# Optimization experiments

Measured on AMD Instinct MI355X. Metric: run time of the kernel, lower is better.

The kernel has to match this reference:

```python
import jax, jax.numpy as jnp
import numpy as np

B, S, D = 4, 2048, 1024
H = 16
DH = D // H  # dim_q = dim_k = 64
F = 4096
EPS = 1e-5


def setup_inputs() -> dict:
    key = jax.random.key(0)
    ks = jax.random.split(key, 16)
    sd = 0.02
    inp = {
        'x': jax.random.normal(ks[0], (B, S, D), jnp.float32),
        'wq': jax.random.normal(ks[1], (H, D, DH), jnp.float32) * sd,
        'bq': jnp.zeros((H, DH), jnp.float32),
        'wk': jax.random.normal(ks[2], (H, D, DH), jnp.float32) * sd,
        'bk': jnp.zeros((H, DH), jnp.float32),
        'wv': jax.random.normal(ks[3], (H, D, DH), jnp.float32) * sd,
        'bv': jnp.zeros((H, DH), jnp.float32),
        'wo': jax.random.normal(ks[4], (H * DH, D), jnp.float32) * sd,
        'bo': jnp.zeros((D,), jnp.float32),
        'ln1_g': jnp.ones((D,), jnp.float32),
        'ln1_b': jnp.zeros((D,), jnp.float32),
        'w1': jax.random.normal(ks[5], (D, F), jnp.float32) * sd,
        'b1': jnp.zeros((F,), jnp.float32),
        'w2': jax.random.normal(ks[6], (F, D), jnp.float32) * sd,
        'b2': jnp.zeros((D,), jnp.float32),
        'ln2_g': jnp.ones((D,), jnp.float32),
        'ln2_b': jnp.zeros((D,), jnp.float32),
    }
    return inp


def _layernorm(x, g, b):
    mu = jnp.mean(x, axis=-1, keepdims=True)
    var = jnp.mean(jnp.square(x - mu), axis=-1, keepdims=True)
    return (x - mu) * jax.lax.rsqrt(var + EPS) * g + b


def _encoder_layer(x, wq, bq, wk, bk, wv, bv, wo, bo, ln1_g, ln1_b,
                   w1, b1, w2, b2, ln2_g, ln2_b):
    # Multi-head attention (all heads batched via einsum)
    q = jnp.einsum('bsd,hde->bhse', x, wq) + bq[:, None, :]
    k = jnp.einsum('bsd,hde->bhse', x, wk) + bk[:, None, :]
    v = jnp.einsum('bsd,hde->bhse', x, wv) + bv[:, None, :]
    scores = jnp.einsum('bhqe,bhke->bhqk', q, k) / jnp.sqrt(jnp.float32(DH))
    p = jax.nn.softmax(scores, axis=-1)
    o = jnp.einsum('bhqk,bhke->bhqe', p, v)  # [B,H,S,DH]
    o = o.transpose(0, 2, 1, 3).reshape(B, S, H * DH)  # concat heads
    attn = o @ wo + bo
    y = _layernorm(x + attn, ln1_g, ln1_b)  # post-norm residual
    # Feed-forward
    ff = jax.nn.relu(y @ w1 + b1) @ w2 + b2
    return _layernorm(y + ff, ln2_g, ln2_b)


def reference(x, wq, bq, wk, bk, wv, bv, wo, bo, ln1_g, ln1_b,
              w1, b1, w2, b2, ln2_g, ln2_b):
    return _encoder_layer(x, wq, bq, wk, bk, wv, bv, wo, bo, ln1_g, ln1_b,
                          w1, b1, w2, b2, ln2_g, ln2_b)
```

## Files before the change

kernel.cpp:

```cpp
#include <hip/hip_runtime.h>
#include <stdint.h>


typedef short bf16x8 __attribute__((ext_vector_type(8)));
typedef unsigned short u16x8 __attribute__((ext_vector_type(8)));
typedef float f32x4 __attribute__((ext_vector_type(4)));
typedef unsigned int u32x2 __attribute__((ext_vector_type(2)));

#define MFMA16(a, b, c) __builtin_amdgcn_mfma_f32_16x16x32_bf16((a), (b), (c), 0, 0, 0)

#define QSCALE 0.1803368801111204f

__device__ __forceinline__ float b2f(unsigned short u) {
    union { unsigned u32; float f; } x;
    x.u32 = ((unsigned)u) << 16;
    return x.f;
}
__device__ __forceinline__ unsigned short f2b(float f) {
    union { float f; unsigned u; } x;
    x.f = f;
    unsigned r = x.u + 0x7fff + ((x.u >> 16) & 1);
    return (unsigned short)(r >> 16);
}

__device__ __forceinline__ void gl16(const unsigned short* g, unsigned short* l) {
    __builtin_amdgcn_global_load_lds(
        (__attribute__((address_space(1))) unsigned int*)(unsigned long)g,
        (__attribute__((address_space(3))) unsigned int*)l, 16, 0, 0);
}

__global__ __launch_bounds__(256) void f2b_bulk(const float* __restrict__ in,
                                                unsigned short* __restrict__ out) {
    const long i = ((long)blockIdx.x * 256 + threadIdx.x) * 8;
    float4 a = *(const float4*)&in[i];
    float4 b = *(const float4*)&in[i + 4];
    u16x8 u;
    u[0] = f2b(a.x); u[1] = f2b(a.y); u[2] = f2b(a.z); u[3] = f2b(a.w);
    u[4] = f2b(b.x); u[5] = f2b(b.y); u[6] = f2b(b.z); u[7] = f2b(b.w);
    *(u16x8*)&out[i] = u;
}

__global__ void transpose_f2b(const float* __restrict__ in,
                              unsigned short* __restrict__ out,
                              int R, int C, long in_batch_stride,
                              int out_row0, int out_ld) {
    __shared__ float tile[32][33];
    const int batch = blockIdx.z;
    const float* src = in + (long)batch * in_batch_stride;
    const int c0 = blockIdx.x * 32, r0 = blockIdx.y * 32;
    const int tx = threadIdx.x, ty = threadIdx.y;
#pragma unroll
    for (int i = 0; i < 32; i += 8)
        tile[ty + i][tx] = src[(long)(r0 + ty + i) * C + c0 + tx];
    __syncthreads();
#pragma unroll
    for (int i = 0; i < 32; i += 8)
        out[(long)(out_row0 + batch * C + c0 + ty + i) * out_ld + r0 + tx] =
            f2b(tile[tx][ty + i]);
}

__global__ void transpose_v(const unsigned short* __restrict__ qkv,
                            unsigned short* __restrict__ vt) {
    __shared__ unsigned short tile[32][33];
    const int bh = blockIdx.z;
    const int b = bh >> 4, h = bh & 15;
    const int s0 = blockIdx.x * 32, e0 = blockIdx.y * 32;
    const int tx = threadIdx.x, ty = threadIdx.y;
    const unsigned short* src = qkv + ((long)b * 2048) * 3072 + 2048 + h * 64;
#pragma unroll
    for (int i = 0; i < 32; i += 8)
        tile[ty + i][tx] = src[(long)(s0 + ty + i) * 3072 + e0 + tx];
    __syncthreads();
    unsigned short* dst = vt + ((long)bh * 64) * 2048;
#pragma unroll
    for (int i = 0; i < 32; i += 8)
        dst[(long)(e0 + ty + i) * 2048 + s0 + tx] = tile[tx][ty + i];
}

__global__ void concat_bias(const float* __restrict__ bq,
                            const float* __restrict__ bk,
                            const float* __restrict__ bv,
                            float* __restrict__ out) {
    int n = blockIdx.x * 256 + threadIdx.x;
    out[n] = (n < 1024) ? bq[n] : (n < 2048) ? bk[n - 1024] : bv[n - 2048];
}

__device__ __forceinline__ float to_f(float v) { return v; }
__device__ __forceinline__ float to_f(unsigned short v) { return b2f(v); }

template <typename RT>
__global__ __launch_bounds__(512, 2) void gemm8p(
    const unsigned short* __restrict__ A, const unsigned short* __restrict__ Bt,
    unsigned short* __restrict__ C, const float* __restrict__ bias,
    const RT* __restrict__ resid, int M, int N, int K, int op) {
    __shared__ __align__(16) unsigned short As[4][128 * 32];
    __shared__ __align__(16) unsigned short Bs[4][256 * 32];
    const int tid = threadIdx.x;
    const int lane = tid & 63;
    const int wave = tid >> 6;
    const int quad = lane >> 4, lr = lane & 15;
    const int wr = wave >> 2, wc = wave & 3;

    const int nx = gridDim.x;
    const int nwg = nx * gridDim.y;
    const int orig = blockIdx.y * nx + blockIdx.x;
    const int wg = (orig & 7) * (nwg >> 3) + (orig >> 3);
    const long n0 = (long)(wg % nx) * 256;
    const long m0 = (long)(wg / nx) * 128;

    f32x4 acc[4][4] = {};

    const int trow = tid >> 2;
    const int tch = ((tid & 3) ^ ((tid >> 3) & 3)) * 8;
    const unsigned short* gA0 = A + (m0 + trow) * (long)K + tch;
    const unsigned short* gB0 = Bt + (n0 + trow) * (long)K + tch;
    const unsigned short* gB1 = Bt + (n0 + 128 + trow) * (long)K + tch;
    unsigned short* const dA = &As[0][0] + tid * 8;
    unsigned short* const dB = &Bs[0][0] + tid * 8;

    int aoff[4], boff[4];
#pragma unroll
    for (int mi = 0; mi < 4; mi++) {
        const int r = wr * 64 + mi * 16 + lr;
        aoff[mi] = r * 32 + (quad ^ ((r >> 1) & 3)) * 8;
    }
#pragma unroll
    for (int ni = 0; ni < 4; ni++) {
        const int r = wc * 64 + ni * 16 + lr;
        boff[ni] = r * 32 + (quad ^ ((r >> 1) & 3)) * 8;
    }

#define G8_STAGE(si, u)                                                   \
    {                                                                     \
        if ((u) == 0)                                                     \
            gl16(gA0 + (long)(si) * 32, dA + ((si) & 3) * 4096);          \
        else if ((u) == 1)                                                \
            gl16(gB0 + (long)(si) * 32, dB + ((si) & 3) * 8192);          \
        else                                                              \
            gl16(gB1 + (long)(si) * 32, dB + ((si) & 3) * 8192 + 4096);   \
    }

    const int S = K >> 5;
    for (int s = 0; s < 3; s++) {
        G8_STAGE(s, 0);
        G8_STAGE(s, 1);
        G8_STAGE(s, 2);
    }
    asm volatile("s_waitcnt vmcnt(6)" ::: "memory");
    __builtin_amdgcn_s_barrier();

    for (int s = 0; s < S; ++s) {
        const int slot = s & 3;
        const unsigned short* as_ = &As[slot][0];
        const unsigned short* bs_ = &Bs[slot][0];
        const bool st = (s + 3) < S;
        bf16x8 af0[2], af1[2], bf0[2], bf1[2];
        af0[0] = *(const bf16x8*)&as_[aoff[0]];
        af0[1] = *(const bf16x8*)&as_[aoff[1]];
        bf0[0] = *(const bf16x8*)&bs_[boff[0]];
        bf0[1] = *(const bf16x8*)&bs_[boff[1]];
        if (st) G8_STAGE(s + 3, 0);
        __builtin_amdgcn_s_barrier();
        asm volatile("s_waitcnt lgkmcnt(0)" ::: "memory");
        __builtin_amdgcn_sched_barrier(0);
        __builtin_amdgcn_s_setprio(1);
        acc[0][0] = MFMA16(af0[0], bf0[0], acc[0][0]);
        acc[0][1] = MFMA16(af0[0], bf0[1], acc[0][1]);
        acc[1][0] = MFMA16(af0[1], bf0[0], acc[1][0]);
        acc[1][1] = MFMA16(af0[1], bf0[1], acc[1][1]);
        __builtin_amdgcn_s_setprio(0);
        __builtin_amdgcn_s_barrier();
        __builtin_amdgcn_sched_barrier(0);
        bf1[0] = *(const bf16x8*)&bs_[boff[2]];
        bf1[1] = *(const bf16x8*)&bs_[boff[3]];
        if (st) G8_STAGE(s + 3, 1);
        __builtin_amdgcn_s_barrier();
        asm volatile("s_waitcnt lgkmcnt(0)" ::: "memory");
        __builtin_amdgcn_sched_barrier(0);
        __builtin_amdgcn_s_setprio(1);
        acc[0][2] = MFMA16(af0[0], bf1[0], acc[0][2]);
        acc[0][3] = MFMA16(af0[0], bf1[1], acc[0][3]);
        acc[1][2] = MFMA16(af0[1], bf1[0], acc[1][2]);
        acc[1][3] = MFMA16(af0[1], bf1[1], acc[1][3]);
        __builtin_amdgcn_s_setprio(0);
        __builtin_amdgcn_s_barrier();
        __builtin_amdgcn_sched_barrier(0);
        af1[0] = *(const bf16x8*)&as_[aoff[2]];
        af1[1] = *(const bf16x8*)&as_[aoff[3]];
        if (st) G8_STAGE(s + 3, 2);
        __builtin_amdgcn_s_barrier();
        asm volatile("s_waitcnt lgkmcnt(0)" ::: "memory");
        __builtin_amdgcn_sched_barrier(0);
        __builtin_amdgcn_s_setprio(1);
        acc[2][2] = MFMA16(af1[0], bf1[0], acc[2][2]);
        acc[2][3] = MFMA16(af1[0], bf1[1], acc[2][3]);
        acc[3][2] = MFMA16(af1[1], bf1[0], acc[3][2]);
        acc[3][3] = MFMA16(af1[1], bf1[1], acc[3][3]);
        __builtin_amdgcn_s_setprio(0);
        __builtin_amdgcn_s_barrier();
        __builtin_amdgcn_sched_barrier(0);
        if (s + 3 < S) {
            asm volatile("s_waitcnt vmcnt(6)" ::: "memory");
        } else if (s + 2 < S) {
            asm volatile("s_waitcnt vmcnt(3)" ::: "memory");
        } else {
            asm volatile("s_waitcnt vmcnt(0)" ::: "memory");
        }
        __builtin_amdgcn_s_barrier();
        __builtin_amdgcn_sched_barrier(0);
        __builtin_amdgcn_s_setprio(1);
        acc[2][0] = MFMA16(af1[0], bf0[0], acc[2][0]);
        acc[2][1] = MFMA16(af1[0], bf0[1], acc[2][1]);
        acc[3][0] = MFMA16(af1[1], bf0[0], acc[3][0]);
        acc[3][1] = MFMA16(af1[1], bf0[1], acc[3][1]);
        __builtin_amdgcn_s_setprio(0);
        __builtin_amdgcn_s_barrier();
        __builtin_amdgcn_sched_barrier(0);
    }
#undef G8_STAGE

#pragma unroll
    for (int ni = 0; ni < 4; ni++) {
        const long col = n0 + wc * 64 + ni * 16 + lr;
        const float bv = bias ? bias[col] : 0.0f;
        const float cscale = (op == 2 && col < 1024) ? QSCALE : 1.0f;
#pragma unroll
        for (int mi = 0; mi < 4; mi++) {
#pragma unroll
            for (int r = 0; r < 4; r++) {
                const long row = m0 + wr * 64 + mi * 16 + quad * 4 + r;
                float v = (acc[mi][ni][r] + bv) * cscale;
                if (resid) v += to_f(resid[row * (long)N + col]);
                if (op == 1) v = fmaxf(v, 0.0f);
                C[row * (long)N + col] = f2b(v);
            }
        }
    }
}

__global__ __launch_bounds__(256, 5) void attn_kernel(
    const unsigned short* __restrict__ qkv, const unsigned short* __restrict__ vt,
    unsigned short* __restrict__ o) {
    __shared__ __align__(16) unsigned short Klds[2][64 * 64];
    __shared__ __align__(16) unsigned short Vlds[2][64 * 64];
    const int l = blockIdx.x;
    const int bh = ((l >> 8) << 3) | (l & 7);
    const int qt = (l >> 3) & 31;
    const int b = bh >> 4, h = bh & 15;
    const int tid = threadIdx.x;
    const int wave = tid >> 6, lane = tid & 63;
    const int quad = lane >> 4, lr = lane & 15;
    const long rowbase = (long)b * 2048;
    const int qb = qt * 64 + wave * 16;

    bf16x8 q0, q1;
    {
        const unsigned short* qrow = qkv + (rowbase + qb + lr) * 3072 + h * 64;
        q0 = *(const bf16x8*)&qrow[quad * 8];
        q1 = *(const bf16x8*)&qrow[32 + quad * 8];
    }

    bf16x8 ones;
#pragma unroll
    for (int i = 0; i < 8; i++) ones[i] = (short)0x3F80;

    const int srow = lane >> 3;
    const int sxc = (lane & 7) ^ srow;
    const unsigned short* kp =
        qkv + (rowbase + wave * 16 + srow) * 3072 + 1024 + h * 64 + sxc * 8;
    const unsigned short* vp =
        vt + ((long)bh * 64 + wave * 16 + srow) * 2048 + sxc * 8;
    const long KADV = 64L * 3072;
    unsigned short* const kd0 = &Klds[0][wave * 16 * 64];
    unsigned short* const vd0 = &Vlds[0][wave * 16 * 64];

#define STAGE(bf)                                                     \
    {                                                                 \
        gl16(kp, kd0 + (bf)*4096);                                    \
        gl16(kp + 8 * 3072, kd0 + (bf)*4096 + 8 * 64);                \
        gl16(vp, vd0 + (bf)*4096);                                    \
        gl16(vp + 8 * 2048, vd0 + (bf)*4096 + 8 * 64);                \
    }

    f32x4 oacc[4] = {};
    f32x4 dacc = {};

    const int x7 = lr & 7;
    const int c00 = (quad ^ x7) * 8;
    const int c01 = ((4 | quad) ^ x7) * 8;

    STAGE(0);
    __syncthreads();

    for (int kt = 0; kt < 32; kt++) {
        const int buf = kt & 1;
        if (kt < 31) {
            kp += KADV;
            vp += 64;
            STAGE(buf ^ 1);
        }
        const unsigned short* kb = &Klds[buf][0];
        f32x4 s4[4];
#pragma unroll
        for (int nt = 0; nt < 4; nt++) {
            const unsigned short* krow = kb + (nt * 16 + lr) * 64;
            bf16x8 k0 = *(const bf16x8*)&krow[c00];
            bf16x8 k1 = *(const bf16x8*)&krow[c01];
            f32x4 z = {};
            z = MFMA16(k0, q0, z);
            z = MFMA16(k1, q1, z);
            s4[nt] = z;
        }
        unsigned pwv[4][2];
#pragma unroll
        for (int nt = 0; nt < 4; nt++) {
            float p0 = exp2f(s4[nt][0]);
            float p1 = exp2f(s4[nt][1]);
            float p2 = exp2f(s4[nt][2]);
            float p3 = exp2f(s4[nt][3]);
            asm("v_cvt_pk_bf16_f32 %0, %1, %2"
                : "=v"(pwv[nt][0]) : "v"(p0), "v"(p1));
            asm("v_cvt_pk_bf16_f32 %0, %1, %2"
                : "=v"(pwv[nt][1]) : "v"(p2), "v"(p3));
        }
        unsigned pq[2][4];
#pragma unroll
        for (int kc = 0; kc < 2; kc++)
#pragma unroll
            for (int tl = 0; tl < 2; tl++) {
                u32x2 y = __builtin_amdgcn_permlane32_swap(
                    pwv[2 * kc][tl], pwv[2 * kc + 1][tl], false, false);
                u32x2 z = __builtin_amdgcn_permlane16_swap(y[0], y[1], false, false);
                pq[kc][tl] = z[0];
                pq[kc][2 + tl] = z[1];
            }

        const unsigned short* vb = &Vlds[buf][0];
#pragma unroll
        for (int kc = 0; kc < 2; kc++) {
            union { unsigned u[4]; bf16x8 h; } pu;
            pu.u[0] = pq[kc][0]; pu.u[1] = pq[kc][1];
            pu.u[2] = pq[kc][2]; pu.u[3] = pq[kc][3];
            const int vc = kc ? c01 : c00;
            dacc = MFMA16(ones, pu.h, dacc);
#pragma unroll
            for (int nt = 0; nt < 4; nt++) {
                bf16x8 va = *(const bf16x8*)&vb[(nt * 16 + lr) * 64 + vc];
                oacc[nt] = MFMA16(va, pu.h, oacc[nt]);
            }
        }
        __syncthreads();
    }

    const float rinv = 1.0f / dacc[0];

    const long orow = rowbase + qb + lr;
#pragma unroll
    for (int nt = 0; nt < 4; nt++) {
        ushort4 ov = {f2b(oacc[nt][0] * rinv), f2b(oacc[nt][1] * rinv),
                      f2b(oacc[nt][2] * rinv), f2b(oacc[nt][3] * rinv)};
        *(ushort4*)&o[orow * 1024 + h * 64 + nt * 16 + quad * 4] = ov;
    }
#undef STAGE
}

__device__ __forceinline__ void st4(float* p, float a, float b, float c, float d) {
    float4 v = {a, b, c, d};
    *(float4*)p = v;
}
__device__ __forceinline__ void st4(unsigned short* p, float a, float b, float c,
                                    float d) {
    ushort4 v = {f2b(a), f2b(b), f2b(c), f2b(d)};
    *(ushort4*)p = v;
}

template <typename OT>
__global__ __launch_bounds__(256) void ln_kernel(
    const unsigned short* __restrict__ in, const float* __restrict__ g,
    const float* __restrict__ b, OT* __restrict__ out) {
    __shared__ float red[4];
    const long row = blockIdx.x;
    const int tid = threadIdx.x;
    ushort4 u = *(const ushort4*)&in[row * 1024 + tid * 4];
    float v[4] = {b2f(u.x), b2f(u.y), b2f(u.z), b2f(u.w)};
    float s = v[0] + v[1] + v[2] + v[3];
#pragma unroll
    for (int off = 32; off > 0; off >>= 1) s += __shfl_down(s, off, 64);
    if ((tid & 63) == 0) red[tid >> 6] = s;
    __syncthreads();
    const float mu = (red[0] + red[1] + red[2] + red[3]) * (1.0f / 1024.0f);
    __syncthreads();
    float d[4], sq = 0.f;
#pragma unroll
    for (int i = 0; i < 4; i++) { d[i] = v[i] - mu; sq += d[i] * d[i]; }
#pragma unroll
    for (int off = 32; off > 0; off >>= 1) sq += __shfl_down(sq, off, 64);
    if ((tid & 63) == 0) red[tid >> 6] = sq;
    __syncthreads();
    const float var = (red[0] + red[1] + red[2] + red[3]) * (1.0f / 1024.0f);
    const float rs = rsqrtf(var + 1e-5f);
    float4 gu = *(const float4*)&g[tid * 4];
    float4 bu = *(const float4*)&b[tid * 4];
    st4(&out[row * 1024 + tid * 4], d[0] * rs * gu.x + bu.x,
        d[1] * rs * gu.y + bu.y, d[2] * rs * gu.z + bu.z,
        d[3] * rs * gu.w + bu.w);
}

extern "C" void kernel_launch(void* const* d_in, const int* in_sizes, int n_in,
                              void* d_out, int out_size, void* d_ws, size_t ws_size,
                              hipStream_t stream) {
    (void)in_sizes; (void)n_in; (void)out_size; (void)ws_size;
    const float* x   = (const float*)d_in[0];
    const float* wq  = (const float*)d_in[1];
    const float* bq  = (const float*)d_in[2];
    const float* wk  = (const float*)d_in[3];
    const float* bk  = (const float*)d_in[4];
    const float* wv  = (const float*)d_in[5];
    const float* bv  = (const float*)d_in[6];
    const float* wo  = (const float*)d_in[7];
    const float* bo  = (const float*)d_in[8];
    const float* g1  = (const float*)d_in[9];
    const float* be1 = (const float*)d_in[10];
    const float* w1  = (const float*)d_in[11];
    const float* b1  = (const float*)d_in[12];
    const float* w2  = (const float*)d_in[13];
    const float* b2  = (const float*)d_in[14];
    const float* g2  = (const float*)d_in[15];
    const float* be2 = (const float*)d_in[16];

    char* ws = (char*)d_ws;
    const size_t MB = 1024 * 1024;
    unsigned short* WT_QKV = (unsigned short*)(ws + 0);
    unsigned short* WT_O   = (unsigned short*)(ws + 6 * MB);
    unsigned short* WT_1   = (unsigned short*)(ws + 8 * MB);
    unsigned short* WT_2   = (unsigned short*)(ws + 16 * MB);
    float*          BQKV   = (float*)(ws + 24 * MB);
    unsigned short* XB     = (unsigned short*)(ws + 25 * MB);
    unsigned short* QKV    = (unsigned short*)(ws + 41 * MB);
    unsigned short* O      = (unsigned short*)(ws + 89 * MB);
    unsigned short* R1     = (unsigned short*)(ws + 25 * MB);
    unsigned short* Y      = (unsigned short*)(ws + 41 * MB);
    unsigned short* R2     = (unsigned short*)(ws + 57 * MB);
    unsigned short* Hb     = (unsigned short*)(ws + 73 * MB);
    unsigned short* VT     = (unsigned short*)(ws + 137 * MB);
    float*          OUT    = (float*)d_out;

    const dim3 tb(32, 8, 1);
    transpose_f2b<<<dim3(2, 32, 16), tb, 0, stream>>>(wq, WT_QKV, 1024, 64, 65536L, 0, 1024);
    transpose_f2b<<<dim3(2, 32, 16), tb, 0, stream>>>(wk, WT_QKV, 1024, 64, 65536L, 1024, 1024);
    transpose_f2b<<<dim3(2, 32, 16), tb, 0, stream>>>(wv, WT_QKV, 1024, 64, 65536L, 2048, 1024);
    transpose_f2b<<<dim3(32, 32, 1), tb, 0, stream>>>(wo, WT_O, 1024, 1024, 0L, 0, 1024);
    transpose_f2b<<<dim3(128, 32, 1), tb, 0, stream>>>(w1, WT_1, 1024, 4096, 0L, 0, 1024);
    transpose_f2b<<<dim3(32, 128, 1), tb, 0, stream>>>(w2, WT_2, 4096, 1024, 0L, 0, 4096);
    concat_bias<<<dim3(12), 256, 0, stream>>>(bq, bk, bv, BQKV);
    f2b_bulk<<<dim3(4096), 256, 0, stream>>>(x, XB);

    gemm8p<unsigned short><<<dim3(12, 64), 512, 0, stream>>>(
        XB, WT_QKV, QKV, BQKV, (const unsigned short*)nullptr, 8192, 3072, 1024, 2);
    transpose_v<<<dim3(64, 2, 64), tb, 0, stream>>>(QKV, VT);
    attn_kernel<<<dim3(2048), 256, 0, stream>>>(QKV, VT, O);
    gemm8p<float><<<dim3(4, 64), 512, 0, stream>>>(
        O, WT_O, R1, bo, x, 8192, 1024, 1024, 0);
    ln_kernel<unsigned short><<<dim3(8192), 256, 0, stream>>>(R1, g1, be1, Y);
    gemm8p<unsigned short><<<dim3(16, 64), 512, 0, stream>>>(
        Y, WT_1, Hb, b1, (const unsigned short*)nullptr, 8192, 4096, 1024, 1);
    gemm8p<unsigned short><<<dim3(4, 64), 512, 0, stream>>>(
        Hb, WT_2, R2, b2, Y, 8192, 1024, 4096, 0);
    ln_kernel<float><<<dim3(8192), 256, 0, stream>>>(R2, g2, be2, OUT);
}
```

Before: 652.8 us.

## Enlarge GEMM block tile to 256x256 with two-phase pipelined k-loop

The GEMM tile grows from 128x256 to 256x256 per workgroup, so each wave now computes a 128x64 sub-tile with 32 accumulators, and the grids halve in the M dimension. The k-loop is restructured into two MFMA phases, each loading A and B fragments and issuing prefetches, with fewer barriers per iteration. This raises arithmetic intensity and cuts global reloads of B, at the cost of doubled LDS (128KB) and more accumulator registers. That may hurt occupancy under launch_bounds(512,2) and leaves fewer workgroups for the small N=1024 GEMMs (128 blocks on 256 CUs).

```diff
diff --git a/kernel.cpp b/kernel.cpp
--- a/kernel.cpp
+++ b/kernel.cpp
@@ -89,11 +89,11 @@
 __device__ __forceinline__ float to_f(unsigned short v) { return b2f(v); }
 
 template <typename RT>
-__global__ __launch_bounds__(512, 2) void gemm8p(
+__global__ __launch_bounds__(512, 2) void gemm256(
     const unsigned short* __restrict__ A, const unsigned short* __restrict__ Bt,
     unsigned short* __restrict__ C, const float* __restrict__ bias,
     const RT* __restrict__ resid, int M, int N, int K, int op) {
-    __shared__ __align__(16) unsigned short As[4][128 * 32];
+    __shared__ __align__(16) unsigned short As[4][256 * 32];
     __shared__ __align__(16) unsigned short Bs[4][256 * 32];
     const int tid = threadIdx.x;
     const int lane = tid & 63;
@@ -106,22 +106,23 @@
     const int orig = blockIdx.y * nx + blockIdx.x;
     const int wg = (orig & 7) * (nwg >> 3) + (orig >> 3);
     const long n0 = (long)(wg % nx) * 256;
-    const long m0 = (long)(wg / nx) * 128;
-
-    f32x4 acc[4][4] = {};
+    const long m0 = (long)(wg / nx) * 256;
+
+    f32x4 acc[8][4] = {};
 
     const int trow = tid >> 2;
     const int tch = ((tid & 3) ^ ((tid >> 3) & 3)) * 8;
     const unsigned short* gA0 = A + (m0 + trow) * (long)K + tch;
+    const unsigned short* gA1 = A + (m0 + 128 + trow) * (long)K + tch;
     const unsigned short* gB0 = Bt + (n0 + trow) * (long)K + tch;
     const unsigned short* gB1 = Bt + (n0 + 128 + trow) * (long)K + tch;
     unsigned short* const dA = &As[0][0] + tid * 8;
     unsigned short* const dB = &Bs[0][0] + tid * 8;
 
-    int aoff[4], boff[4];
-#pragma unroll
-    for (int mi = 0; mi < 4; mi++) {
-        const int r = wr * 64 + mi * 16 + lr;
+    int aoff[8], boff[4];
+#pragma unroll
+    for (int mi = 0; mi < 8; mi++) {
+        const int r = wr * 128 + mi * 16 + lr;
         aoff[mi] = r * 32 + (quad ^ ((r >> 1) & 3)) * 8;
     }
 #pragma unroll
@@ -130,23 +131,23 @@
         boff[ni] = r * 32 + (quad ^ ((r >> 1) & 3)) * 8;
     }
 
-#define G8_STAGE(si, u)                                                   \
-    {                                                                     \
-        if ((u) == 0)                                                     \
-            gl16(gA0 + (long)(si) * 32, dA + ((si) & 3) * 4096);          \
-        else if ((u) == 1)                                                \
-            gl16(gB0 + (long)(si) * 32, dB + ((si) & 3) * 8192);          \
-        else                                                              \
-            gl16(gB1 + (long)(si) * 32, dB + ((si) & 3) * 8192 + 4096);   \
+#define STAGE_A(si)                                                   \
+    {                                                                 \
+        gl16(gA0 + (long)(si) * 32, dA + ((si) & 3) * 8192);          \
+        gl16(gA1 + (long)(si) * 32, dA + ((si) & 3) * 8192 + 4096);   \
+    }
+#define STAGE_B(si)                                                   \
+    {                                                                 \
+        gl16(gB0 + (long)(si) * 32, dB + ((si) & 3) * 8192);          \
+        gl16(gB1 + (long)(si) * 32, dB + ((si) & 3) * 8192 + 4096);   \
     }
 
     const int S = K >> 5;
     for (int s = 0; s < 3; s++) {
-        G8_STAGE(s, 0);
-        G8_STAGE(s, 1);
-        G8_STAGE(s, 2);
-    }
-    asm volatile("s_waitcnt vmcnt(6)" ::: "memory");
+        STAGE_A(s);
+        STAGE_B(s);
+    }
+    asm volatile("s_waitcnt vmcnt(8)" ::: "memory");
     __builtin_amdgcn_s_barrier();
 
     for (int s = 0; s < S; ++s) {
@@ -154,70 +155,49 @@
         const unsigned short* as_ = &As[slot][0];
         const unsigned short* bs_ = &Bs[slot][0];
         const bool st = (s + 3) < S;
-        bf16x8 af0[2], af1[2], bf0[2], bf1[2];
-        af0[0] = *(const bf16x8*)&as_[aoff[0]];
-        af0[1] = *(const bf16x8*)&as_[aoff[1]];
-        bf0[0] = *(const bf16x8*)&bs_[boff[0]];
-        bf0[1] = *(const bf16x8*)&bs_[boff[1]];
-        if (st) G8_STAGE(s + 3, 0);
+        bf16x8 af[8], bf[4];
+#pragma unroll
+        for (int mi = 0; mi < 8; mi++) af[mi] = *(const bf16x8*)&as_[aoff[mi]];
+        bf[0] = *(const bf16x8*)&bs_[boff[0]];
+        bf[1] = *(const bf16x8*)&bs_[boff[1]];
+        if (st) STAGE_A(s + 3);
         __builtin_amdgcn_s_barrier();
         asm volatile("s_waitcnt lgkmcnt(0)" ::: "memory");
         __builtin_amdgcn_sched_barrier(0);
         __builtin_amdgcn_s_setprio(1);
-        acc[0][0] = MFMA16(af0[0], bf0[0], acc[0][0]);
-        acc[0][1] = MFMA16(af0[0], bf0[1], acc[0][1]);
-        acc[1][0] = MFMA16(af0[1], bf0[0], acc[1][0]);
-        acc[1][1] = MFMA16(af0[1], bf0[1], acc[1][1]);
+#pragma unroll
+        for (int mi = 0; mi < 8; mi++) {
+            acc[mi][0] = MFMA16(af[mi], bf[0], acc[mi][0]);
+            acc[mi][1] = MFMA16(af[mi], bf[1], acc[mi][1]);
+        }
         __builtin_amdgcn_s_setprio(0);
         __builtin_amdgcn_s_barrier();
         __builtin_amdgcn_sched_barrier(0);
-        bf1[0] = *(const bf16x8*)&bs_[boff[2]];
-        bf1[1] = *(const bf16x8*)&bs_[boff[3]];
-        if (st) G8_STAGE(s + 3, 1);
+        bf[2] = *(const bf16x8*)&bs_[boff[2]];
+        bf[3] = *(const bf16x8*)&bs_[boff[3]];
+        if (st) STAGE_B(s + 3);
         __builtin_amdgcn_s_barrier();
         asm volatile("s_waitcnt lgkmcnt(0)" ::: "memory");
         __builtin_amdgcn_sched_barrier(0);
         __builtin_amdgcn_s_setprio(1);
-        acc[0][2] = MFMA16(af0[0], bf1[0], acc[0][2]);
-        acc[0][3] = MFMA16(af0[0], bf1[1], acc[0][3]);
-        acc[1][2] = MFMA16(af0[1], bf1[0], acc[1][2]);
-        acc[1][3] = MFMA16(af0[1], bf1[1], acc[1][3]);
+#pragma unroll
+        for (int mi = 0; mi < 8; mi++) {
+            acc[mi][2] = MFMA16(af[mi], bf[2], acc[mi][2]);
+            acc[mi][3] = MFMA16(af[mi], bf[3], acc[mi][3]);
+        }
         __builtin_amdgcn_s_setprio(0);
+        if (s + 3 < S) {
+            asm volatile("s_waitcnt vmcnt(8)" ::: "memory");
+        } else if (s + 2 < S) {
+            asm volatile("s_waitcnt vmcnt(4)" ::: "memory");
+        } else {
+            asm volatile("s_waitcnt vmcnt(0)" ::: "memory");
+        }
         __builtin_amdgcn_s_barrier();
         __builtin_amdgcn_sched_barrier(0);
-        af1[0] = *(const bf16x8*)&as_[aoff[2]];
-        af1[1] = *(const bf16x8*)&as_[aoff[3]];
-        if (st) G8_STAGE(s + 3, 2);
-        __builtin_amdgcn_s_barrier();
-        asm volatile("s_waitcnt lgkmcnt(0)" ::: "memory");
-        __builtin_amdgcn_sched_barrier(0);
-        __builtin_amdgcn_s_setprio(1);
-        acc[2][2] = MFMA16(af1[0], bf1[0], acc[2][2]);
-        acc[2][3] = MFMA16(af1[0], bf1[1], acc[2][3]);
-        acc[3][2] = MFMA16(af1[1], bf1[0], acc[3][2]);
-        acc[3][3] = MFMA16(af1[1], bf1[1], acc[3][3]);
-        __builtin_amdgcn_s_setprio(0);
-        __builtin_amdgcn_s_barrier();
-        __builtin_amdgcn_sched_barrier(0);
-        if (s + 3 < S) {
-            asm volatile("s_waitcnt vmcnt(6)" ::: "memory");
-        } else if (s + 2 < S) {
-            asm volatile("s_waitcnt vmcnt(3)" ::: "memory");
-        } else {
-            asm volatile("s_waitcnt vmcnt(0)" ::: "memory");
-        }
-        __builtin_amdgcn_s_barrier();
-        __builtin_amdgcn_sched_barrier(0);
-        __builtin_amdgcn_s_setprio(1);
-        acc[2][0] = MFMA16(af1[0], bf0[0], acc[2][0]);
-        acc[2][1] = MFMA16(af1[0], bf0[1], acc[2][1]);
-        acc[3][0] = MFMA16(af1[1], bf0[0], acc[3][0]);
-        acc[3][1] = MFMA16(af1[1], bf0[1], acc[3][1]);
-        __builtin_amdgcn_s_setprio(0);
-        __builtin_amdgcn_s_barrier();
-        __builtin_amdgcn_sched_barrier(0);
-    }
-#undef G8_STAGE
+    }
+#undef STAGE_A
+#undef STAGE_B
 
 #pragma unroll
     for (int ni = 0; ni < 4; ni++) {
@@ -225,10 +205,10 @@
         const float bv = bias ? bias[col] : 0.0f;
         const float cscale = (op == 2 && col < 1024) ? QSCALE : 1.0f;
 #pragma unroll
-        for (int mi = 0; mi < 4; mi++) {
+        for (int mi = 0; mi < 8; mi++) {
 #pragma unroll
             for (int r = 0; r < 4; r++) {
-                const long row = m0 + wr * 64 + mi * 16 + quad * 4 + r;
+                const long row = m0 + wr * 128 + mi * 16 + quad * 4 + r;
                 float v = (acc[mi][ni][r] + bv) * cscale;
                 if (resid) v += to_f(resid[row * (long)N + col]);
                 if (op == 1) v = fmaxf(v, 0.0f);
@@ -455,16 +435,16 @@
     concat_bias<<<dim3(12), 256, 0, stream>>>(bq, bk, bv, BQKV);
     f2b_bulk<<<dim3(4096), 256, 0, stream>>>(x, XB);
 
-    gemm8p<unsigned short><<<dim3(12, 64), 512, 0, stream>>>(
+    gemm256<unsigned short><<<dim3(12, 32), 512, 0, stream>>>(
         XB, WT_QKV, QKV, BQKV, (const unsigned short*)nullptr, 8192, 3072, 1024, 2);
     transpose_v<<<dim3(64, 2, 64), tb, 0, stream>>>(QKV, VT);
     attn_kernel<<<dim3(2048), 256, 0, stream>>>(QKV, VT, O);
-    gemm8p<float><<<dim3(4, 64), 512, 0, stream>>>(
+    gemm256<float><<<dim3(4, 32), 512, 0, stream>>>(
         O, WT_O, R1, bo, x, 8192, 1024, 1024, 0);
     ln_kernel<unsigned short><<<dim3(8192), 256, 0, stream>>>(R1, g1, be1, Y);
-    gemm8p<unsigned short><<<dim3(16, 64), 512, 0, stream>>>(
+    gemm256<unsigned short><<<dim3(16, 32), 512, 0, stream>>>(
         Y, WT_1, Hb, b1, (const unsigned short*)nullptr, 8192, 4096, 1024, 1);
-    gemm8p<unsigned short><<<dim3(4, 64), 512, 0, stream>>>(
+    gemm256<unsigned short><<<dim3(4, 32), 512, 0, stream>>>(
         Hb, WT_2, R2, b2, Y, 8192, 1024, 4096, 0);
     ln_kernel<float><<<dim3(8192), 256, 0, stream>>>(R2, g2, be2, OUT);
 }
```

Result: slower. 669.0 us (+2.5%).
